# Optimization experiments

Measured on AMD Instinct MI355X. Metric: run time of the kernel, lower is better.

The kernel has to match this reference:

```python
import jax, jax.numpy as jnp
import numpy as np

N = 4096      # nnode
F = 128       # feature_dim
E = 64        # embed_dim
P_EDGE = 0.01 # edge probability (~41 avg degree)
NEG = -9e15
ALPHA = 0.2   # leaky relu slope


def _xavier(key, shape):
    lim = float(np.sqrt(6.0 / (shape[0] + shape[1])))
    return jax.random.uniform(key, shape, minval=-lim, maxval=lim, dtype=jnp.float32)


def setup_inputs() -> dict:
    key = jax.random.key(0)
    ks = jax.random.split(key, 14)
    features = jax.random.normal(ks[0], (N, F), dtype=jnp.float32)
    eye = jnp.eye(N, dtype=jnp.float32)

    def make_adj(k):
        a = (jax.random.uniform(k, (N, N)) < P_EDGE).astype(jnp.float32)
        return jnp.maximum(a, eye)  # self loop so no empty rows

    return {
        "features": features,
        "geo_adj": make_adj(ks[1]),
        "forward_adj": make_adj(ks[2]),
        "backward_adj": make_adj(ks[3]),
        "weight": _xavier(ks[4], (E, F)),
        "Wf": _xavier(ks[5], (F, E)),
        "af1": jax.random.normal(ks[6], (E,), dtype=jnp.float32) * 0.1,
        "af2": jax.random.normal(ks[7], (E,), dtype=jnp.float32) * 0.1,
        "Wb": _xavier(ks[8], (F, E)),
        "ab1": jax.random.normal(ks[9], (E,), dtype=jnp.float32) * 0.1,
        "ab2": jax.random.normal(ks[10], (E,), dtype=jnp.float32) * 0.1,
        "Wg": _xavier(ks[11], (F, E)),
        "ag1": jax.random.normal(ks[12], (E,), dtype=jnp.float32) * 0.1,
        "ag2": jax.random.normal(ks[13], (E,), dtype=jnp.float32) * 0.1,
    }


def _mean_neighbors(adj, feat):
    # pre_weight: row-normalized neighbor averaging, (N,N) @ (N,F)
    deg = jnp.clip(jnp.sum(adj, axis=1, keepdims=True), 1.0, None)
    return (adj @ feat) / deg


def _attention(feat, mask_feat, adj, W, a1, a2):
    # GAT-style additive attention with masked softmax over neighbors
    h = feat @ W        # (N, E)
    hm = mask_feat @ W  # (N, E)
    e = jax.nn.leaky_relu((h @ a1)[:, None] + (hm @ a2)[None, :], negative_slope=ALPHA)  # (N, N)
    e = jnp.where(adj > 0, e, NEG)
    return jax.nn.softmax(e, axis=1)  # (N, N)


def reference(features, geo_adj, forward_adj, backward_adj, weight,
              Wf, af1, af2, Wb, ab1, ab2, Wg, ag1, ag2):
    t = features  # (N, F)
    mask_f = _mean_neighbors(forward_adj, t)
    mask_b = _mean_neighbors(backward_adj, t)
    mask_g = _mean_neighbors(geo_adj, t)

    w_f = _attention(t, mask_f, forward_adj, Wf, af1, af2)
    w_b = _attention(t, mask_b, backward_adj, Wb, ab1, ab2)
    w_g = _attention(t, mask_g, geo_adj, Wg, ag1, ag2)

    # get_mask_matrix_i/_j broadcast-mul + sum(1) == attn @ t (or attn.T @ t)
    x = weight @ t.T                  # (E, N)
    x_fwd = weight @ (w_f @ t).T      # mask_matrix_i
    x_bwd = weight @ (w_b.T @ t).T    # mask_matrix_j (transposed)
    x_geo = weight @ (w_g @ t).T      # mask_matrix_i

    return jnp.concatenate([x, x_fwd, x_bwd, x_geo], axis=0)  # (4E, N)
```

## Files before the change

kernel.cpp:

```cpp
#include <hip/hip_runtime.h>

#define NN 4096
#define FF 128
#define EE 64

typedef unsigned short u16;
typedef unsigned long long u64;
typedef float vf4 __attribute__((ext_vector_type(4)));

__device__ __forceinline__ float lrelu(float x) { return x > 0.f ? x : 0.2f * x; }

__global__ void k_prep(const float* __restrict__ Wf, const float* __restrict__ af1, const float* __restrict__ af2,
                       const float* __restrict__ Wb, const float* __restrict__ ab1, const float* __restrict__ ab2,
                       const float* __restrict__ Wg, const float* __restrict__ ag1, const float* __restrict__ ag2,
                       float* __restrict__ v6)
{
    const float* Ws[3]  = {Wf, Wb, Wg};
    const float* a1s[3] = {af1, ab1, ag1};
    const float* a2s[3] = {af2, ab2, ag2};
    int vi = blockIdx.x, f = threadIdx.x, dd = vi >> 1;
    const float* a = (vi & 1) ? a2s[dd] : a1s[dd];
    const float* W = Ws[dd] + (size_t)f * EE;
    float s = 0.f;
    #pragma unroll 8
    for (int e = 0; e < EE; ++e) s += W[e] * a[e];
    v6[vi * FF + f] = s;
}

__global__ __launch_bounds__(256)
void k_feat(const float* __restrict__ t, const float* __restrict__ weight,
            const float* __restrict__ v6,
            float* __restrict__ u, float* __restrict__ s1, float* __restrict__ p,
            float* __restrict__ out, int* __restrict__ ccnt)
{
    __shared__ float ww[64 * 129];
    __shared__ float tt[16 * 130];
    __shared__ float vv[6 * FF];
    __shared__ float uacc[64 * 17];
    int b = blockIdx.x, tid = threadIdx.x;
    int n0 = b * 16;
    if (b < 16) ccnt[b * 256 + tid] = 0;
    const float4* w4 = reinterpret_cast<const float4*>(weight);
    for (int i = tid; i < 2048; i += 256) {
        float4 v = w4[i];
        int fi = i * 4, e = fi >> 7, q = fi & 127;
        float* dst = &ww[e * 129 + q];
        dst[0] = v.x; dst[1] = v.y; dst[2] = v.z; dst[3] = v.w;
    }
    const float4* t4 = reinterpret_cast<const float4*>(t + (size_t)n0 * FF);
    for (int i = tid; i < 512; i += 256) {
        float4 v = t4[i];
        int fi = i * 4, nd = fi >> 7, q = fi & 127;
        float* dst = &tt[nd * 130 + q];
        dst[0] = v.x; dst[1] = v.y; dst[2] = v.z; dst[3] = v.w;
    }
    for (int i = tid; i < 6 * FF; i += 256) vv[i] = v6[i];
    __syncthreads();
    int g = tid >> 6, lane = tid & 63;
    for (int k = 0; k < 4; ++k) {
        int nd = g * 4 + k;
        const float* trow = &tt[nd * 130];
        const float* wrow = &ww[lane * 129];
        float acc = 0.f;
        #pragma unroll 16
        for (int q = 0; q < 128; ++q) acc += wrow[q] * trow[q];
        u[(size_t)(n0 + nd) * EE + lane] = acc;
        uacc[lane * 17 + nd] = acc;
        float t0 = trow[lane], t1 = trow[64 + lane];
        for (int vi = 0; vi < 6; ++vi) {
            float x = t0 * vv[vi * FF + lane] + t1 * vv[vi * FF + 64 + lane];
            for (int off = 32; off; off >>= 1) x += __shfl_xor(x, off);
            if (lane == 0) {
                int dd = vi >> 1;
                if (vi & 1) p[dd * NN + n0 + nd] = x; else s1[dd * NN + n0 + nd] = x;
            }
        }
    }
    __syncthreads();
    int e = tid >> 2, io = (tid & 3) * 4;
    float* orow = out + (size_t)e * NN + n0 + io;
    orow[0] = uacc[e * 17 + io];
    orow[1] = uacc[e * 17 + io + 1];
    orow[2] = uacc[e * 17 + io + 2];
    orow[3] = uacc[e * 17 + io + 3];
}

__global__ __launch_bounds__(256, 8)
void k_scan(const float* __restrict__ Af, const float* __restrict__ Ab, const float* __restrict__ Ag,
            const float* __restrict__ p,
            u16* __restrict__ csr, int* __restrict__ cnt, float* __restrict__ s2,
            u16* __restrict__ csc, int* __restrict__ ccnt, int stride)
{
    int wid = threadIdx.x >> 6, lane = threadIdx.x & 63;
    int gr = blockIdx.x * 4 + wid;
    int d = gr >> 12, r = gr & (NN - 1);
    const float* A = d == 0 ? Af : (d == 1 ? Ab : Ag);
    const vf4* row4 = reinterpret_cast<const vf4*>(A + (size_t)r * NN);
    const float* pd = p + d * NN;

    u64 mask = 0ull;
    #pragma unroll
    for (int j = 0; j < 16; ++j) {
        vf4 L = __builtin_nontemporal_load(row4 + j * 64 + lane);
        unsigned mm = (L.x != 0.f ? 1u : 0u) | (L.y != 0.f ? 2u : 0u) |
                      (L.z != 0.f ? 4u : 0u) | (L.w != 0.f ? 8u : 0u);
        mask |= ((u64)mm) << (j * 4);
    }

    int lc = __popcll(mask);
    int sc = lc;
    for (int off = 1; off < 64; off <<= 1) {
        int o = __shfl_up(sc, off);
        if (lane >= off) sc += o;
    }
    int total = __shfl(sc, 63);
    int pos = sc - lc;
    u16* crow = csr + (size_t)gr * stride;
    float q = 0.f;
    u64 m = mask;
    while (m) {
        int b = __ffsll(m) - 1;
        m &= m - 1;
        int col = ((b >> 2) << 8) + (lane << 2) + (b & 3);
        if (pos < stride) crow[pos] = (u16)col;
        pos++;
        q += pd[col];
        if (d == 1) {
            int cp = atomicAdd(&ccnt[col], 1);
            if (cp < stride) csc[(size_t)col * stride + cp] = (u16)r;
        }
    }
    for (int off = 32; off; off >>= 1) q += __shfl_xor(q, off);
    if (lane == 0) {
        cnt[gr] = total;
        s2[gr] = q / fmaxf((float)total, 1.f);
    }
}

__global__ void k_zb(const float* __restrict__ s1, const float* __restrict__ s2,
                     const u16* __restrict__ csr, const int* __restrict__ cnt, int stride,
                     float* __restrict__ Zb)
{
    int tid = threadIdx.x, wave = tid >> 6, lane = tid & 63;
    int j = blockIdx.x * 4 + wave;
    int gr = NN + j;
    int nnz = min(cnt[gr], stride);
    const u16* crow = csr + (size_t)gr * stride;
    float s1j = s1[gr];
    const float* s2b = s2 + NN;
    float z = 0.f;
    if (lane < nnz)      z += __expf(lrelu(s1j + s2b[crow[lane]]));
    if (lane + 64 < nnz) z += __expf(lrelu(s1j + s2b[crow[lane + 64]]));
    for (int off = 32; off; off >>= 1) z += __shfl_xor(z, off);
    if (lane == 0) Zb[j] = z;
}

__global__ __launch_bounds__(256)
void k_out(const float* __restrict__ u,
           const float* __restrict__ s1, const float* __restrict__ s2,
           const float* __restrict__ Zb,
           const u16* __restrict__ csr, const int* __restrict__ cnt,
           const u16* __restrict__ csc, const int* __restrict__ ccnt, int stride,
           float* __restrict__ out)
{
    __shared__ float oacc[16 * 66];
    int gr0 = blockIdx.x * 16;
    int d = gr0 >> 12, i0 = gr0 & (NN - 1);
    int wid = threadIdx.x >> 6, lane = threadIdx.x & 63;
    for (int k = 0; k < 4; ++k) {
        int lr = k * 4 + wid;
        int i = i0 + lr;
        int gr = gr0 + lr;
        int nnz;
        int c0v = 0, c1v = 0;
        float w0v = 0.f, w1v = 0.f;
        if (d == 1) {
            nnz = min(ccnt[i], stride);
            const u16* cc = csc + (size_t)i * stride;
            float s2i = s2[NN + i];
            if (lane < nnz)      { int j = cc[lane];      c0v = j; w0v = __expf(lrelu(s1[NN + j] + s2i)) / Zb[j]; }
            if (lane + 64 < nnz) { int j = cc[lane + 64]; c1v = j; w1v = __expf(lrelu(s1[NN + j] + s2i)) / Zb[j]; }
        } else {
            nnz = min(cnt[gr], stride);
            const u16* crow = csr + (size_t)gr * stride;
            float s1i = s1[gr];
            const float* s2d = s2 + d * NN;
            float z = 0.f;
            if (lane < nnz)      { int c = crow[lane];      c0v = c; w0v = __expf(lrelu(s1i + s2d[c])); z += w0v; }
            if (lane + 64 < nnz) { int c = crow[lane + 64]; c1v = c; w1v = __expf(lrelu(s1i + s2d[c])); z += w1v; }
            for (int off = 32; off; off >>= 1) z += __shfl_xor(z, off);
            float invz = z > 0.f ? 1.f / z : 0.f;
            w0v *= invz; w1v *= invz;
        }
        float a0 = 0.f, a1 = 0.f;
        int n0 = nnz < 64 ? nnz : 64;
        int kk = 0;
        for (; kk + 1 < n0; kk += 2) {
            int ca = __shfl(c0v, kk), cb = __shfl(c0v, kk + 1);
            float wa = __shfl(w0v, kk), wb = __shfl(w0v, kk + 1);
            a0 += wa * u[(size_t)ca * EE + lane];
            a1 += wb * u[(size_t)cb * EE + lane];
        }
        if (kk < n0)
            a0 += __shfl(w0v, kk) * u[(size_t)__shfl(c0v, kk) * EE + lane];
        int n1 = nnz - 64;
        kk = 0;
        for (; kk + 1 < n1; kk += 2) {
            int ca = __shfl(c1v, kk), cb = __shfl(c1v, kk + 1);
            float wa = __shfl(w1v, kk), wb = __shfl(w1v, kk + 1);
            a0 += wa * u[(size_t)ca * EE + lane];
            a1 += wb * u[(size_t)cb * EE + lane];
        }
        if (kk < n1)
            a0 += __shfl(w1v, kk) * u[(size_t)__shfl(c1v, kk) * EE + lane];
        oacc[lr * 66 + lane] = a0 + a1;
    }
    __syncthreads();
    int e = threadIdx.x >> 2, io = (threadIdx.x & 3) * 4;
    int base = 64 + (d << 6);
    float* orow = out + (size_t)(base + e) * NN + i0 + io;
    orow[0] = oacc[(io    ) * 66 + e];
    orow[1] = oacc[(io + 1) * 66 + e];
    orow[2] = oacc[(io + 2) * 66 + e];
    orow[3] = oacc[(io + 3) * 66 + e];
}

extern "C" void kernel_launch(void* const* d_in, const int* in_sizes, int n_in,
                              void* d_out, int out_size, void* d_ws, size_t ws_size,
                              hipStream_t stream)
{
    const float* t   = (const float*)d_in[0];
    const float* Ag  = (const float*)d_in[1];
    const float* Af  = (const float*)d_in[2];
    const float* Ab  = (const float*)d_in[3];
    const float* W   = (const float*)d_in[4];
    const float* Wf  = (const float*)d_in[5];
    const float* af1 = (const float*)d_in[6];
    const float* af2 = (const float*)d_in[7];
    const float* Wb  = (const float*)d_in[8];
    const float* ab1 = (const float*)d_in[9];
    const float* ab2 = (const float*)d_in[10];
    const float* Wg  = (const float*)d_in[11];
    const float* ag1 = (const float*)d_in[12];
    const float* ag2 = (const float*)d_in[13];
    float* out = (float*)d_out;

    float* ws = (float*)d_ws;
    float* v6  = ws;
    float* s1  = v6 + 6 * FF;
    float* p   = s1 + 3 * NN;
    float* s2  = p + 3 * NN;
    float* Zb  = s2 + 3 * NN;
    float* u   = Zb + NN;
    int*   cnt  = (int*)(u + (size_t)NN * EE);
    int*   ccnt = cnt + 3 * NN;
    u16*   csr  = (u16*)(ccnt + NN);

    size_t base_bytes = ((char*)csr) - ((char*)d_ws);
    int stride = 128;
    if (base_bytes + (size_t)4 * NN * 128 * 2 > ws_size) stride = 96;
    if (base_bytes + (size_t)4 * NN * 96 * 2 > ws_size)  stride = 64;
    u16* csc = csr + (size_t)3 * NN * stride;

    k_prep<<<6, 128, 0, stream>>>(Wf, af1, af2, Wb, ab1, ab2, Wg, ag1, ag2, v6);
    k_feat<<<NN / 16, 256, 0, stream>>>(t, W, v6, u, s1, p, out, ccnt);
    k_scan<<<3 * NN / 4, 256, 0, stream>>>(Af, Ab, Ag, p, csr, cnt, s2, csc, ccnt, stride);
    k_zb<<<NN / 4, 256, 0, stream>>>(s1, s2, csr, cnt, stride, Zb);
    k_out<<<3 * NN / 16, 256, 0, stream>>>(u, s1, s2, Zb, csr, cnt, csc, ccnt, stride, out);
}
```

Before: 254.5 us.

## Fuse prep into feature kernel, interleave scan rows across graphs, unroll gather

Merges the tiny W·a projection kernel into the feature kernel. 64 extra blocks recompute the six projected vectors and produce s1/p directly, while the remaining blocks compute u and the first output rows. The scan kernel now interleaves rows of the three adjacency matrices across consecutive waves, which spreads atomics and mixes memory streams. The gather loop in k_out is unrolled to four independent accumulators for more memory-level parallelism. This saves one launch and shortens reduction chains. In exchange, each of the 64 prep blocks redundantly recomputes the 768 dot products.

```diff
diff --git a/kernel.cpp b/kernel.cpp
--- a/kernel.cpp
+++ b/kernel.cpp
@@ -10,36 +10,57 @@
 
 __device__ __forceinline__ float lrelu(float x) { return x > 0.f ? x : 0.2f * x; }
 
-__global__ void k_prep(const float* __restrict__ Wf, const float* __restrict__ af1, const float* __restrict__ af2,
-                       const float* __restrict__ Wb, const float* __restrict__ ab1, const float* __restrict__ ab2,
-                       const float* __restrict__ Wg, const float* __restrict__ ag1, const float* __restrict__ ag2,
-                       float* __restrict__ v6)
-{
-    const float* Ws[3]  = {Wf, Wb, Wg};
-    const float* a1s[3] = {af1, ab1, ag1};
-    const float* a2s[3] = {af2, ab2, ag2};
-    int vi = blockIdx.x, f = threadIdx.x, dd = vi >> 1;
-    const float* a = (vi & 1) ? a2s[dd] : a1s[dd];
-    const float* W = Ws[dd] + (size_t)f * EE;
-    float s = 0.f;
-    #pragma unroll 8
-    for (int e = 0; e < EE; ++e) s += W[e] * a[e];
-    v6[vi * FF + f] = s;
-}
-
 __global__ __launch_bounds__(256)
-void k_feat(const float* __restrict__ t, const float* __restrict__ weight,
-            const float* __restrict__ v6,
-            float* __restrict__ u, float* __restrict__ s1, float* __restrict__ p,
-            float* __restrict__ out, int* __restrict__ ccnt)
+void k_pre(const float* __restrict__ t, const float* __restrict__ weight,
+           const float* __restrict__ Wf, const float* __restrict__ af1, const float* __restrict__ af2,
+           const float* __restrict__ Wb, const float* __restrict__ ab1, const float* __restrict__ ab2,
+           const float* __restrict__ Wg, const float* __restrict__ ag1, const float* __restrict__ ag2,
+           float* __restrict__ u, float* __restrict__ s1, float* __restrict__ p,
+           float* __restrict__ out, int* __restrict__ ccnt)
 {
     __shared__ float ww[64 * 129];
     __shared__ float tt[16 * 130];
-    __shared__ float vv[6 * FF];
     __shared__ float uacc[64 * 17];
+    __shared__ float w6[6 * FF];
     int b = blockIdx.x, tid = threadIdx.x;
-    int n0 = b * 16;
-    if (b < 16) ccnt[b * 256 + tid] = 0;
+
+    if (b < 64) {
+        if (b < 16) ccnt[b * 256 + tid] = 0;
+        const float* Ws[3]  = {Wf, Wb, Wg};
+        const float* a1s[3] = {af1, ab1, ag1};
+        const float* a2s[3] = {af2, ab2, ag2};
+        for (int idx = tid; idx < 768; idx += 256) {
+            int vi = idx >> 7, f = idx & 127, dd = vi >> 1;
+            const float4* a4 = reinterpret_cast<const float4*>((vi & 1) ? a2s[dd] : a1s[dd]);
+            const float4* W4 = reinterpret_cast<const float4*>(Ws[dd] + (size_t)f * EE);
+            float s = 0.f;
+            #pragma unroll
+            for (int e4 = 0; e4 < 16; ++e4) {
+                float4 wv = W4[e4], av = a4[e4];
+                s += wv.x * av.x + wv.y * av.y + wv.z * av.z + wv.w * av.w;
+            }
+            w6[vi * FF + f] = s;
+        }
+        __syncthreads();
+        int nb = b * 64;
+        for (int idx = tid; idx < 384; idx += 256) {
+            int n = idx & 63, vi = idx >> 6;
+            const float4* t4 = reinterpret_cast<const float4*>(t + (size_t)(nb + n) * FF);
+            const float* wv = &w6[vi * FF];
+            float s = 0.f;
+            #pragma unroll 8
+            for (int q4 = 0; q4 < 32; ++q4) {
+                float4 v = t4[q4];
+                s += v.x * wv[q4 * 4] + v.y * wv[q4 * 4 + 1]
+                   + v.z * wv[q4 * 4 + 2] + v.w * wv[q4 * 4 + 3];
+            }
+            int dd = vi >> 1;
+            if (vi & 1) p[dd * NN + nb + n] = s; else s1[dd * NN + nb + n] = s;
+        }
+        return;
+    }
+
+    int n0 = (b - 64) * 16;
     const float4* w4 = reinterpret_cast<const float4*>(weight);
     for (int i = tid; i < 2048; i += 256) {
         float4 v = w4[i];
@@ -54,7 +75,6 @@
         float* dst = &tt[nd * 130 + q];
         dst[0] = v.x; dst[1] = v.y; dst[2] = v.z; dst[3] = v.w;
     }
-    for (int i = tid; i < 6 * FF; i += 256) vv[i] = v6[i];
     __syncthreads();
     int g = tid >> 6, lane = tid & 63;
     for (int k = 0; k < 4; ++k) {
@@ -66,15 +86,6 @@
         for (int q = 0; q < 128; ++q) acc += wrow[q] * trow[q];
         u[(size_t)(n0 + nd) * EE + lane] = acc;
         uacc[lane * 17 + nd] = acc;
-        float t0 = trow[lane], t1 = trow[64 + lane];
-        for (int vi = 0; vi < 6; ++vi) {
-            float x = t0 * vv[vi * FF + lane] + t1 * vv[vi * FF + 64 + lane];
-            for (int off = 32; off; off >>= 1) x += __shfl_xor(x, off);
-            if (lane == 0) {
-                int dd = vi >> 1;
-                if (vi & 1) p[dd * NN + n0 + nd] = x; else s1[dd * NN + n0 + nd] = x;
-            }
-        }
     }
     __syncthreads();
     int e = tid >> 2, io = (tid & 3) * 4;
@@ -92,8 +103,9 @@
             u16* __restrict__ csc, int* __restrict__ ccnt, int stride)
 {
     int wid = threadIdx.x >> 6, lane = threadIdx.x & 63;
-    int gr = blockIdx.x * 4 + wid;
-    int d = gr >> 12, r = gr & (NN - 1);
+    int gl = blockIdx.x * 4 + wid;
+    int d = gl % 3, r = gl / 3;
+    int gr = d * NN + r;
     const float* A = d == 0 ? Af : (d == 1 ? Ab : Ag);
     const vf4* row4 = reinterpret_cast<const vf4*>(A + (size_t)r * NN);
     const float* pd = p + d * NN;
@@ -119,9 +131,9 @@
     float q = 0.f;
     u64 m = mask;
     while (m) {
-        int b = __ffsll(m) - 1;
+        int bb = __ffsll(m) - 1;
         m &= m - 1;
-        int col = ((b >> 2) << 8) + (lane << 2) + (b & 3);
+        int col = ((bb >> 2) << 8) + (lane << 2) + (bb & 3);
         if (pos < stride) crow[pos] = (u16)col;
         pos++;
         q += pd[col];
@@ -192,28 +204,36 @@
             float invz = z > 0.f ? 1.f / z : 0.f;
             w0v *= invz; w1v *= invz;
         }
-        float a0 = 0.f, a1 = 0.f;
-        int n0 = nnz < 64 ? nnz : 64;
+        float a0 = 0.f, a1 = 0.f, a2 = 0.f, a3 = 0.f;
+        int n0c = nnz < 64 ? nnz : 64;
         int kk = 0;
-        for (; kk + 1 < n0; kk += 2) {
-            int ca = __shfl(c0v, kk), cb = __shfl(c0v, kk + 1);
-            float wa = __shfl(w0v, kk), wb = __shfl(w0v, kk + 1);
-            a0 += wa * u[(size_t)ca * EE + lane];
-            a1 += wb * u[(size_t)cb * EE + lane];
-        }
-        if (kk < n0)
+        for (; kk + 3 < n0c; kk += 4) {
+            int ca = __shfl(c0v, kk),     cb = __shfl(c0v, kk + 1);
+            int cc2 = __shfl(c0v, kk + 2), cd = __shfl(c0v, kk + 3);
+            float wa = __shfl(w0v, kk),     wb = __shfl(w0v, kk + 1);
+            float wc = __shfl(w0v, kk + 2), wd = __shfl(w0v, kk + 3);
+            a0 += wa * u[(size_t)ca  * EE + lane];
+            a1 += wb * u[(size_t)cb  * EE + lane];
+            a2 += wc * u[(size_t)cc2 * EE + lane];
+            a3 += wd * u[(size_t)cd  * EE + lane];
+        }
+        for (; kk < n0c; ++kk)
             a0 += __shfl(w0v, kk) * u[(size_t)__shfl(c0v, kk) * EE + lane];
-        int n1 = nnz - 64;
+        int n1c = nnz - 64;
         kk = 0;
-        for (; kk + 1 < n1; kk += 2) {
-            int ca = __shfl(c1v, kk), cb = __shfl(c1v, kk + 1);
-            float wa = __shfl(w1v, kk), wb = __shfl(w1v, kk + 1);
-            a0 += wa * u[(size_t)ca * EE + lane];
-            a1 += wb * u[(size_t)cb * EE + lane];
-        }
-        if (kk < n1)
+        for (; kk + 3 < n1c; kk += 4) {
+            int ca = __shfl(c1v, kk),     cb = __shfl(c1v, kk + 1);
+            int cc2 = __shfl(c1v, kk + 2), cd = __shfl(c1v, kk + 3);
+            float wa = __shfl(w1v, kk),     wb = __shfl(w1v, kk + 1);
+            float wc = __shfl(w1v, kk + 2), wd = __shfl(w1v, kk + 3);
+            a0 += wa * u[(size_t)ca  * EE + lane];
+            a1 += wb * u[(size_t)cb  * EE + lane];
+            a2 += wc * u[(size_t)cc2 * EE + lane];
+            a3 += wd * u[(size_t)cd  * EE + lane];
+        }
+        for (; kk < n1c; ++kk)
             a0 += __shfl(w1v, kk) * u[(size_t)__shfl(c1v, kk) * EE + lane];
-        oacc[lr * 66 + lane] = a0 + a1;
+        oacc[lr * 66 + lane] = (a0 + a1) + (a2 + a3);
     }
     __syncthreads();
     int e = threadIdx.x >> 2, io = (threadIdx.x & 3) * 4;
@@ -262,8 +282,8 @@
     if (base_bytes + (size_t)4 * NN * 96 * 2 > ws_size)  stride = 64;
     u16* csc = csr + (size_t)3 * NN * stride;
 
-    k_prep<<<6, 128, 0, stream>>>(Wf, af1, af2, Wb, ab1, ab2, Wg, ag1, ag2, v6);
-    k_feat<<<NN / 16, 256, 0, stream>>>(t, W, v6, u, s1, p, out, ccnt);
+    k_pre<<<320, 256, 0, stream>>>(t, W, Wf, af1, af2, Wb, ab1, ab2, Wg, ag1, ag2,
+                                   u, s1, p, out, ccnt);
     k_scan<<<3 * NN / 4, 256, 0, stream>>>(Af, Ab, Ag, p, csr, cnt, s2, csc, ccnt, stride);
     k_zb<<<NN / 4, 256, 0, stream>>>(s1, s2, csr, cnt, stride, Zb);
     k_out<<<3 * NN / 16, 256, 0, stream>>>(u, s1, s2, Zb, csr, cnt, csc, ccnt, stride, out);
```

Measured after the change: 246.5 us. 1.03x faster.
